# Kernel tuning notes

Measured on AMD Instinct MI355X. Metric: run time of the kernel, lower is better.

Reference implementation:

```python
import jax, jax.numpy as jnp
import numpy as np

H = 16          # num_heads
HD = 64         # head_dim = latent_dim // num_heads
RHD = 32        # rope_head_dim = head_dim // 2
NHD = 32        # nope_head_dim
Q_LAT = 256     # latent_dim // compression_ratio
KV_LAT = 204    # xf_latent_dim // (compression_ratio + 1)
MAX_LEN = 2048
THETA = 10000.0
EPS = 1e-5


def _rope_tables():
    half = RHD // 2  # 16
    freqs = 1.0 / THETA ** (np.arange(half, dtype=np.float32) / half)
    t = np.arange(MAX_LEN, dtype=np.float32)
    ang = np.outer(t, freqs)  # (MAX_LEN, half)
    return jnp.asarray(np.cos(ang)), jnp.asarray(np.sin(ang))

COS, SIN = _rope_tables()


def _ln(x, g, b):
    m = jnp.mean(x, axis=-1, keepdims=True)
    v = jnp.var(x, axis=-1, keepdims=True)
    return (x - m) * jax.lax.rsqrt(v + EPS) * g + b


def _rope(t, cos, sin):
    # t: (..., L, RHD); cos/sin: (L, RHD//2); interleaved even/odd convention
    ev, od = t[..., 0::2], t[..., 1::2]
    oe = ev * cos - od * sin
    oo = ev * sin + od * cos
    return jnp.stack([oe, oo], axis=-1).reshape(t.shape)


def setup_inputs() -> dict:
    key = jax.random.key(0)
    ks = jax.random.split(key, 12)
    D = 1024
    s = 0.02
    return {
        "x": jax.random.normal(ks[0], (2, 2048, D), jnp.float32),
        "xf": jax.random.normal(ks[1], (2, 2048, D), jnp.float32),
        "Wqc": jax.random.normal(ks[2], (D, Q_LAT), jnp.float32) * s,
        "gq": jnp.ones((Q_LAT,), jnp.float32),
        "bq": jnp.zeros((Q_LAT,), jnp.float32),
        "Wq_rope": jax.random.normal(ks[3], (Q_LAT, H * RHD), jnp.float32) * s,
        "Wq_nope": jax.random.normal(ks[4], (Q_LAT, H * NHD), jnp.float32) * s,
        "Wkvc": jax.random.normal(ks[5], (D, KV_LAT), jnp.float32) * s,
        "gkv": jnp.ones((KV_LAT,), jnp.float32),
        "bkv": jnp.zeros((KV_LAT,), jnp.float32),
        "Wk_nope": jax.random.normal(ks[6], (KV_LAT, H * NHD), jnp.float32) * s,
        "Wv": jax.random.normal(ks[7], (KV_LAT, H * HD), jnp.float32) * s,
        "Wkr": jax.random.normal(ks[8], (D, RHD), jnp.float32) * s,
        "Wo": jax.random.normal(ks[9], (D, D), jnp.float32) * s,
        "bo": jnp.zeros((D,), jnp.float32),
    }


def reference(x, xf, Wqc, gq, bq, Wq_rope, Wq_nope, Wkvc, gkv, bkv, Wk_nope, Wv, Wkr, Wo, bo):
    B, T, D = x.shape
    S = xf.shape[1]

    # query path: compress -> LN -> decoupled decompress
    ql = _ln(x @ Wqc, gq, bq)                                   # (B,T,Q_LAT)
    q_nope = (ql @ Wq_nope).reshape(B, T, H, NHD).transpose(0, 2, 1, 3)  # (B,H,T,NHD)
    q_rope = (ql @ Wq_rope).reshape(B, T, H, RHD).transpose(0, 2, 1, 3)  # (B,H,T,RHD)

    # key/value path: compress -> LN -> decompress; shared single rope head
    kvl = _ln(xf @ Wkvc, gkv, bkv)                              # (B,S,KV_LAT)
    k_nope = (kvl @ Wk_nope).reshape(B, S, H, NHD).transpose(0, 2, 1, 3)  # (B,H,S,NHD)
    v = (kvl @ Wv).reshape(B, S, H, HD).transpose(0, 2, 1, 3)   # (B,H,S,HD)
    k_rope = (xf @ Wkr).reshape(B, S, 1, RHD).transpose(0, 2, 1, 3)       # (B,1,S,RHD)

    q_rope = _rope(q_rope, COS[:T], SIN[:T])
    k_rope = _rope(k_rope, COS[:S], SIN[:S]) / H
    k_rope = jnp.broadcast_to(k_rope, (B, H, S, RHD))

    q = jnp.concatenate([q_nope, q_rope], axis=-1)              # (B,H,T,HD)
    k = jnp.concatenate([k_nope, k_rope], axis=-1)              # (B,H,S,HD)

    scale = 1.0 / jnp.sqrt(jnp.asarray(HD, q.dtype))
    scores = jnp.einsum("bhtd,bhsd->bhts", q, k) * scale
    attn = jax.nn.softmax(scores, axis=-1)
    o = jnp.einsum("bhts,bhsd->bhtd", attn, v)                  # (B,H,T,HD)
    o = o.transpose(0, 2, 1, 3).reshape(B, T, H * HD)
    return o @ Wo + bo
```

## Files before the change

### kernel.cpp

```cpp
#include <hip/hip_runtime.h>
#include <hip/hip_bf16.h>
#include <math.h>

#define SEQ 2048

typedef __bf16 bf16x8 __attribute__((ext_vector_type(8)));
typedef float  f32x4  __attribute__((ext_vector_type(4)));

#if __has_builtin(__builtin_amdgcn_exp2f)
#define EXP2(x) __builtin_amdgcn_exp2f(x)
#else
#define EXP2(x) exp2f(x)
#endif

__device__ __forceinline__ unsigned short f2bf(float f) {
  __bf16 h = (__bf16)f;
  return __builtin_bit_cast(unsigned short, h);
}

__device__ __forceinline__ void gload16(const unsigned short* g, unsigned short* l) {
  __builtin_amdgcn_global_load_lds(
      (const __attribute__((address_space(1))) void*)g,
      (__attribute__((address_space(3))) void*)l, 16, 0, 0);
}

__device__ __forceinline__ unsigned cvtpk(float lo, float hi) {
  unsigned r;
  asm("v_cvt_pk_bf16_f32 %0, %1, %2" : "=v"(r) : "v"(lo), "v"(hi));
  return r;
}
__device__ __forceinline__ void plswap32(unsigned &a, unsigned &b) {
  asm("v_permlane32_swap_b32 %0, %1" : "+v"(a), "+v"(b));
}
__device__ __forceinline__ void plswap16(unsigned &a, unsigned &b) {
  asm("v_permlane16_swap_b32 %0, %1" : "+v"(a), "+v"(b));
}

#define CLOG (0.125f * 1.44269504f)

struct WPrep {
  const float* src[8];
  unsigned short* dst[8];
  int K[8], N[8], NR[8], KC[8], nb[8];
  float2* cst;
};

__global__ __launch_bounds__(256) void wprep_kernel(WPrep p)
{
  __shared__ float tile[32][33];
  int bid = blockIdx.x;
  if (bid < 128) {
    const int idx = bid * 256 + threadIdx.x;
    const int pos = idx >> 4, i = idx & 15;
    const float freq = EXP2(-(float)i * 0.8304820237f);
    const float ang = (float)pos * freq;
    p.cst[idx] = make_float2(cosf(ang), sinf(ang));
    return;
  }
  bid -= 128;
  int di = 0;
  while (bid >= p.nb[di]) { bid -= p.nb[di]; ++di; }
  const float* src = p.src[di];
  unsigned short* dst = p.dst[di];
  const int K = p.K[di], N = p.N[di], KC = p.KC[di];
  const int nkx = KC >> 5;
  const int k0 = (bid % nkx) * 32, n0 = (bid / nkx) * 32;
  const int tx = threadIdx.x & 31, ty = threadIdx.x >> 5;
  for (int r = ty; r < 32; r += 8) {
    const int k = k0 + r, n = n0 + tx;
    tile[r][tx] = (k < K && n < N) ? src[(long)k * N + n] : 0.0f;
  }
  __syncthreads();
  for (int r = ty; r < 32; r += 8) {
    const int n = n0 + r, k = k0 + tx;
    dst[(long)n * KC + k] = f2bf(tile[tx][r]);
  }
}

template <int EPI, bool AF32>
__device__ __forceinline__ void gemm_body(
    unsigned short* smem,
    const void* __restrict__ Av, const unsigned short* __restrict__ BT,
    const float* __restrict__ bias, const float2* __restrict__ cst,
    void* __restrict__ C0v, void* __restrict__ C1v, int K, int N,
    int bx, int by)
{
  unsigned short* As = smem;
  unsigned short* Bs = smem + 2 * 128 * 32;
  const int tid = threadIdx.x;
  const int w = tid >> 6, lane = tid & 63;
  const int ln16 = lane & 15, quad = lane >> 4;
  const int wm = (w >> 1) * 64, wn = (w & 1) * 64;
  const int m0 = by * 128, n0 = bx * 128;
  const int rr = tid >> 2, cc = (tid & 3) * 8;

  const unsigned short* A = (const unsigned short*)Av;

  auto stageB = [&](int ib, int k0) {
    gload16(&BT[(long)(n0 + rr)      * K + k0 + cc], &Bs[ib * 4096 + rr * 32 + cc]);
    gload16(&BT[(long)(n0 + 64 + rr) * K + k0 + cc], &Bs[ib * 4096 + (64 + rr) * 32 + cc]);
  };
  auto stageAbf = [&](int ib, int k0) {
    gload16(&A[(long)(m0 + rr)      * K + k0 + cc], &As[ib * 4096 + rr * 32 + cc]);
    gload16(&A[(long)(m0 + 64 + rr) * K + k0 + cc], &As[ib * 4096 + (64 + rr) * 32 + cc]);
  };

  f32x4 acc[4][4];
#pragma unroll
  for (int i = 0; i < 4; ++i)
#pragma unroll
    for (int j = 0; j < 4; ++j)
#pragma unroll
      for (int r = 0; r < 4; ++r) acc[i][j][r] = 0.0f;

  stageB(0, 0);
  stageAbf(0, 0);

  int ib = 0;
  for (int k0 = 0; k0 < K; k0 += 32, ib ^= 1) {
    __syncthreads();
    const int kn = k0 + 32;
    if (kn < K) { stageB(ib ^ 1, kn); stageAbf(ib ^ 1, kn); }
    bf16x8 fa[4], fb[4];
#pragma unroll
    for (int i = 0; i < 4; ++i) fa[i] = *(const bf16x8*)&As[ib * 4096 + (wm + i * 16 + ln16) * 32 + quad * 8];
#pragma unroll
    for (int j = 0; j < 4; ++j) fb[j] = *(const bf16x8*)&Bs[ib * 4096 + (wn + j * 16 + ln16) * 32 + quad * 8];
#pragma unroll
    for (int i = 0; i < 4; ++i)
#pragma unroll
      for (int j = 0; j < 4; ++j)
        acc[i][j] = __builtin_amdgcn_mfma_f32_16x16x32_bf16(fa[i], fb[j], acc[i][j], 0, 0, 0);
  }

  if (EPI == 5 && n0 >= 512) {
    __syncthreads();
#pragma unroll
    for (int i = 0; i < 4; ++i) {
      const int rl = wm + i * 16 + quad * 4;
#pragma unroll
      for (int j = 0; j < 4; ++j) {
        const int cl = wn + j * 16 + ln16;
        ushort4 u;
        u.x = f2bf(acc[i][j][0]); u.y = f2bf(acc[i][j][1]);
        u.z = f2bf(acc[i][j][2]); u.w = f2bf(acc[i][j][3]);
        *(ushort4*)&smem[cl * 132 + rl] = u;
      }
    }
    __syncthreads();
    unsigned short* vT = (unsigned short*)C1v;
    const int b = m0 >> 11, sbase = m0 & (SEQ - 1);
    for (int q = tid; q < 128 * 16; q += 256) {
      const int cl = q >> 4, sch = (q & 15) * 8;
      bf16x8 val = *(const bf16x8*)&smem[cl * 132 + sch];
      const int c = (n0 - 512) + cl;
      const int hh = c >> 6, dd = c & 63;
      *(bf16x8*)&vT[((long)(b * 16 + hh) * 64 + dd) * SEQ + sbase + sch] = val;
    }
    return;
  }
#pragma unroll
  for (int i = 0; i < 4; ++i) {
    const int row0 = m0 + wm + i * 16 + quad * 4;
#pragma unroll
    for (int j = 0; j < 4; ++j) {
      const int col = n0 + wn + j * 16 + ln16;
      if (EPI == 3) {
        if (n0 < 512) {
          unsigned short* qn = (unsigned short*)C0v;
#pragma unroll
          for (int r = 0; r < 4; ++r) qn[(long)(row0 + r) * 512 + col] = f2bf(acc[i][j][r] * CLOG);
        } else {
          unsigned short* qr = (unsigned short*)C1v;
          const int c = col - 512;
          const int d = c & 31;
#pragma unroll
          for (int r = 0; r < 4; ++r) {
            const float v = acc[i][j][r];
            const float p = __shfl_xor(v, 1);
            const float2 t = cst[((row0 + r) & (SEQ - 1)) * 16 + (d >> 1)];
            const float o = ((d & 1) == 0) ? (v * t.x - p * t.y) : (p * t.y + v * t.x);
            qr[(long)(row0 + r) * 512 + c] = f2bf(o * CLOG);
          }
        }
      } else if (EPI == 5) {
        unsigned short* kn = (unsigned short*)C0v;
#pragma unroll
        for (int r = 0; r < 4; ++r) kn[(long)(row0 + r) * 512 + col] = f2bf(acc[i][j][r]);
      }
    }
  }
}

template <int E0, bool AF0, int E1, bool AF1>
__global__ __launch_bounds__(256) void gemm_dual(
    const void* __restrict__ A0, const unsigned short* __restrict__ BT0,
    void* __restrict__ C00, void* __restrict__ C01, int K0, int N0, int nx0,
    const void* __restrict__ A1, const unsigned short* __restrict__ BT1,
    void* __restrict__ C10, void* __restrict__ C11, int K1, int N1,
    const float2* __restrict__ cst)
{
  __shared__ unsigned short smem[16896];
  if (blockIdx.z == 0) {
    if ((int)blockIdx.x >= nx0) return;
    gemm_body<E0, AF0>(smem, A0, BT0, nullptr, cst, C00, C01, K0, N0, blockIdx.x, blockIdx.y);
  } else {
    gemm_body<E1, AF1>(smem, A1, BT1, nullptr, cst, C10, C11, K1, N1, blockIdx.x, blockIdx.y);
  }
}

template <int EPI, bool AF32>
__device__ __forceinline__ void gemm_body64(
    unsigned short* smem,
    const void* __restrict__ Av, const unsigned short* __restrict__ BT,
    const float* __restrict__ bias, const float2* __restrict__ cst,
    void* __restrict__ C0v, void* __restrict__ C1v, int K, int N,
    int bx, int by)
{
  unsigned short* As = smem;
  unsigned short* Bs = smem + 2 * 64 * 32;
  const int tid = threadIdx.x;
  const int w = tid >> 6, lane = tid & 63;
  const int ln16 = lane & 15, quad = lane >> 4;
  const int wm = (w >> 1) * 32, wn = (w & 1) * 32;
  const int m0 = by * 64, n0 = bx * 64;
  const int rr = tid >> 2, cc = (tid & 3) * 8;

  const unsigned short* A = (const unsigned short*)Av;
  const float* Af = (const float*)Av;

  auto stageB = [&](int ib, int k0) {
    gload16(&BT[(long)(n0 + rr) * K + k0 + cc], &Bs[ib * 2048 + rr * 32 + cc]);
  };
  auto stageAbf = [&](int ib, int k0) {
    gload16(&A[(long)(m0 + rr) * K + k0 + cc], &As[ib * 2048 + rr * 32 + cc]);
  };
  auto writeAf32 = [&](int ib, const float4& a0, const float4& a1) {
    ushort4 u;
    u.x = f2bf(a0.x); u.y = f2bf(a0.y); u.z = f2bf(a0.z); u.w = f2bf(a0.w);
    *(ushort4*)&As[ib * 2048 + rr * 32 + cc] = u;
    u.x = f2bf(a1.x); u.y = f2bf(a1.y); u.z = f2bf(a1.z); u.w = f2bf(a1.w);
    *(ushort4*)&As[ib * 2048 + rr * 32 + cc + 4] = u;
  };

  f32x4 acc[2][2];
#pragma unroll
  for (int i = 0; i < 2; ++i)
#pragma unroll
    for (int j = 0; j < 2; ++j)
#pragma unroll
      for (int r = 0; r < 4; ++r) acc[i][j][r] = 0.0f;

  stageB(0, 0);
  if (AF32) {
    float4 a0 = *(const float4*)&Af[(long)(m0 + rr) * K + cc];
    float4 a1 = *(const float4*)&Af[(long)(m0 + rr) * K + cc + 4];
    writeAf32(0, a0, a1);
  } else {
    stageAbf(0, 0);
  }

  int ib = 0;
  for (int k0 = 0; k0 < K; k0 += 32, ib ^= 1) {
    __syncthreads();
    const int kn = k0 + 32;
    float4 a0, a1;
    if (kn < K) {
      stageB(ib ^ 1, kn);
      if (AF32) {
        a0 = *(const float4*)&Af[(long)(m0 + rr) * K + kn + cc];
        a1 = *(const float4*)&Af[(long)(m0 + rr) * K + kn + cc + 4];
      } else {
        stageAbf(ib ^ 1, kn);
      }
    }
    bf16x8 fa[2], fb[2];
#pragma unroll
    for (int i = 0; i < 2; ++i) fa[i] = *(const bf16x8*)&As[ib * 2048 + (wm + i * 16 + ln16) * 32 + quad * 8];
#pragma unroll
    for (int j = 0; j < 2; ++j) fb[j] = *(const bf16x8*)&Bs[ib * 2048 + (wn + j * 16 + ln16) * 32 + quad * 8];
#pragma unroll
    for (int i = 0; i < 2; ++i)
#pragma unroll
      for (int j = 0; j < 2; ++j)
        acc[i][j] = __builtin_amdgcn_mfma_f32_16x16x32_bf16(fa[i], fb[j], acc[i][j], 0, 0, 0);
    if (AF32 && kn < K) writeAf32(ib ^ 1, a0, a1);
  }

#pragma unroll
  for (int i = 0; i < 2; ++i) {
    const int row0 = m0 + wm + i * 16 + quad * 4;
#pragma unroll
    for (int j = 0; j < 2; ++j) {
      const int col = n0 + wn + j * 16 + ln16;
      if (EPI == 0 || EPI == 1) {
        float* C = (float*)C0v;
        float bv = (EPI == 1) ? bias[col] : 0.0f;
#pragma unroll
        for (int r = 0; r < 4; ++r) C[(long)(row0 + r) * N + col] = acc[i][j][r] + bv;
      } else if (EPI == 4) {
        if (n0 < 256) {
          float* kvl = (float*)C0v;
#pragma unroll
          for (int r = 0; r < 4; ++r) kvl[(long)(row0 + r) * 256 + col] = acc[i][j][r];
        } else if (wn == 0) {
          unsigned short* kr = (unsigned short*)C1v;
          const int d = col - 256;
#pragma unroll
          for (int r = 0; r < 4; ++r) {
            const float v = acc[i][j][r];
            const float p = __shfl_xor(v, 1);
            const float2 t = cst[((row0 + r) & (SEQ - 1)) * 16 + (d >> 1)];
            const float o = ((d & 1) == 0) ? (v * t.x - p * t.y) : (p * t.y + v * t.x);
            kr[(long)(row0 + r) * 32 + d] = f2bf(o * 0.0625f);
          }
        }
      }
    }
  }
}

template <int EPI, bool AF32>
__global__ __launch_bounds__(256) void gemm_mfma64(
    const void* __restrict__ Av, const unsigned short* __restrict__ BT,
    const float* __restrict__ bias, const float2* __restrict__ cst,
    void* __restrict__ C0v, void* __restrict__ C1v, int K, int N)
{
  __shared__ unsigned short smem[8192];
  gemm_body64<EPI, AF32>(smem, Av, BT, bias, cst, C0v, C1v, K, N, blockIdx.x, blockIdx.y);
}

template <int E0, bool AF0, int E1, bool AF1>
__global__ __launch_bounds__(256) void gemm_dual64(
    const void* __restrict__ A0, const unsigned short* __restrict__ BT0,
    void* __restrict__ C00, void* __restrict__ C01, int K0, int N0, int nx0,
    const void* __restrict__ A1, const unsigned short* __restrict__ BT1,
    void* __restrict__ C10, void* __restrict__ C11, int K1, int N1,
    const float2* __restrict__ cst)
{
  __shared__ unsigned short smem[8192];
  if (blockIdx.z == 0) {
    if ((int)blockIdx.x >= nx0) return;
    gemm_body64<E0, AF0>(smem, A0, BT0, nullptr, cst, C00, C01, K0, N0, blockIdx.x, blockIdx.y);
  } else {
    gemm_body64<E1, AF1>(smem, A1, BT1, nullptr, cst, C10, C11, K1, N1, blockIdx.x, blockIdx.y);
  }
}

__global__ __launch_bounds__(256) void ln2_kernel(
    const float* __restrict__ Xq, const float* __restrict__ Xkv,
    const float* __restrict__ gq, const float* __restrict__ bq,
    const float* __restrict__ gkv, const float* __restrict__ bkv,
    unsigned short* __restrict__ Yq, unsigned short* __restrict__ Ykv)
{
  const int row0 = blockIdx.x, tid = threadIdx.x;
  const bool isq = row0 < 4096;
  const int row = isq ? row0 : row0 - 4096;
  const float* X = isq ? Xq : Xkv;
  const float* g = isq ? gq : gkv;
  const float* b = isq ? bq : bkv;
  unsigned short* Y = isq ? Yq : Ykv;
  const int C = isq ? 256 : 204;
  const int Cp = isq ? 256 : 224;
  float v = (tid < C) ? X[(long)row * 256 + tid] : 0.0f;
  float s1 = v, s2 = v * v;
#pragma unroll
  for (int off = 1; off < 64; off <<= 1) {
    s1 += __shfl_xor(s1, off);
    s2 += __shfl_xor(s2, off);
  }
  __shared__ float rA[4], rB[4];
  const int wid = tid >> 6;
  if ((tid & 63) == 0) { rA[wid] = s1; rB[wid] = s2; }
  __syncthreads();
  s1 = rA[0] + rA[1] + rA[2] + rA[3];
  s2 = rB[0] + rB[1] + rB[2] + rB[3];
  const float mean = s1 / C;
  const float var  = s2 / C - mean * mean;
  const float r = rsqrtf(var + 1e-5f);
  if (tid < C) Y[(long)row * Cp + tid] = f2bf((v - mean) * r * g[tid] + b[tid]);
  else if (tid < Cp) Y[(long)row * Cp + tid] = 0;
}

#define KSTR 36
#define VSTR 68
__global__ __launch_bounds__(256, 4) void attn_mfma_kernel(
    const unsigned short* __restrict__ qn, const unsigned short* __restrict__ qr,
    const unsigned short* __restrict__ kn, const unsigned short* __restrict__ kr,
    const unsigned short* __restrict__ vT, unsigned short* __restrict__ ob)
{
  __shared__ unsigned short Kn[2][64 * KSTR];
  __shared__ unsigned short Vs[2][64 * VSTR];
  const int id = blockIdx.x;
  const int xcd = id & 7, j = id >> 3;
  const int bh = xcd * 4 + (j & 3);
  const int tile = j >> 2;
  const int b = bh >> 4, h = bh & 15;
  const int t0 = tile * 64;
  const int tid = threadIdx.x;
  const int w = tid >> 6, lane = tid & 63;
  const int ln16 = lane & 15, quad = lane >> 4;
  const int trow = w * 16;
  const long bT = (long)b * SEQ;

  const int krow = tid >> 2, kc8 = (tid & 3) * 8;
  const int vd0 = tid >> 3, vc0 = (tid & 7) * 8;
  const int vd1 = vd0 + 32;

  bf16x8 q0 = *(const bf16x8*)&qn[(bT + t0 + trow + ln16) * 512 + h * 32 + quad * 8];
  bf16x8 q1 = *(const bf16x8*)&qr[(bT + t0 + trow + ln16) * 512 + h * 32 + quad * 8];

  auto loadKV = [&](int s0, bf16x8& rk0, bf16x8& rv0, bf16x8& rv1) {
    rk0 = *(const bf16x8*)&kn[(bT + s0 + krow) * 512 + h * 32 + kc8];
    rv0 = *(const bf16x8*)&vT[((long)bh * 64 + vd0) * SEQ + s0 + vc0];
    rv1 = *(const bf16x8*)&vT[((long)bh * 64 + vd1) * SEQ + s0 + vc0];
  };
  auto writeKV = [&](int ib, bf16x8 rk0, bf16x8 rv0, bf16x8 rv1) {
    *(bf16x8*)&Kn[ib][krow * KSTR + kc8] = rk0;
    *(bf16x8*)&Vs[ib][vd0 * VSTR + vc0] = rv0;
    *(bf16x8*)&Vs[ib][vd1 * VSTR + vc0] = rv1;
  };
  auto loadKrF = [&](int s0, bf16x8* f) {
#pragma unroll
    for (int nt = 0; nt < 4; ++nt)
      f[nt] = *(const bf16x8*)&kr[(bT + s0 + nt * 16 + ln16) * 32 + quad * 8];
  };

  bf16x8 ck0, cv0, cv1;
  bf16x8 nk0, nv0, nv1;
  bf16x8 ckr[4], nkr[4];
  loadKV(0, ck0, cv0, cv1);
  writeKV(0, ck0, cv0, cv1);
  loadKV(64, nk0, nv0, nv1);
  loadKrF(0, ckr);
  loadKrF(64, nkr);

  f32x4 o_acc[4];
#pragma unroll
  for (int nt = 0; nt < 4; ++nt)
#pragma unroll
    for (int r = 0; r < 4; ++r) o_acc[nt][r] = 0.0f;
  float l_part = 0.0f;

  int ib = 0;
  for (int s0 = 0; s0 < SEQ; s0 += 64, ib ^= 1) {
    __syncthreads();
    if (s0 + 64 < SEQ) {
      writeKV(ib ^ 1, nk0, nv0, nv1);
      if (s0 + 128 < SEQ) loadKV(s0 + 128, nk0, nv0, nv1);
    }

    f32x4 sf[4];
#pragma unroll
    for (int nt = 0; nt < 4; ++nt)
#pragma unroll
      for (int r = 0; r < 4; ++r) sf[nt][r] = 0.0f;
#pragma unroll
    for (int nt = 0; nt < 4; ++nt) {
      bf16x8 a0 = *(const bf16x8*)&Kn[ib][(nt * 16 + ln16) * KSTR + quad * 8];
      sf[nt] = __builtin_amdgcn_mfma_f32_16x16x32_bf16(a0, q0, sf[nt], 0, 0, 0);
      sf[nt] = __builtin_amdgcn_mfma_f32_16x16x32_bf16(ckr[nt], q1, sf[nt], 0, 0, 0);
    }

#pragma unroll
    for (int nt = 0; nt < 4; ++nt) ckr[nt] = nkr[nt];
    if (s0 + 128 < SEQ) loadKrF(s0 + 128, nkr);

    unsigned u0, u1, u2, u3, u4, u5, u6, u7;
    {
      float p[16];
#pragma unroll
      for (int nt = 0; nt < 4; ++nt)
#pragma unroll
        for (int r = 0; r < 4; ++r) {
          const float e = EXP2(sf[nt][r]);
          p[nt * 4 + r] = e;
          l_part += e;
        }
      u0 = cvtpk(p[0],  p[1]);   u1 = cvtpk(p[2],  p[3]);
      u2 = cvtpk(p[4],  p[5]);   u3 = cvtpk(p[6],  p[7]);
      u4 = cvtpk(p[8],  p[9]);   u5 = cvtpk(p[10], p[11]);
      u6 = cvtpk(p[12], p[13]);  u7 = cvtpk(p[14], p[15]);
    }
    plswap32(u0, u2); plswap16(u0, u2);
    plswap32(u1, u3); plswap16(u1, u3);
    plswap32(u4, u6); plswap16(u4, u6);
    plswap32(u5, u7); plswap16(u5, u7);
    const uint4 w0 = make_uint4(u0, u1, u2, u3);
    const uint4 w1 = make_uint4(u4, u5, u6, u7);
    bf16x8 a0 = __builtin_bit_cast(bf16x8, w0);
    bf16x8 a1 = __builtin_bit_cast(bf16x8, w1);

#pragma unroll
    for (int nt = 0; nt < 4; ++nt) {
      bf16x8 v0 = *(const bf16x8*)&Vs[ib][(nt * 16 + ln16) * VSTR + quad * 8];
      o_acc[nt] = __builtin_amdgcn_mfma_f32_16x16x32_bf16(a0, v0, o_acc[nt], 0, 0, 0);
      bf16x8 v1 = *(const bf16x8*)&Vs[ib][(nt * 16 + ln16) * VSTR + 32 + quad * 8];
      o_acc[nt] = __builtin_amdgcn_mfma_f32_16x16x32_bf16(a1, v1, o_acc[nt], 0, 0, 0);
    }
  }

  float l_i = l_part;
  l_i += __shfl_xor(l_i, 16);
  l_i += __shfl_xor(l_i, 32);
  const float lr = 1.0f / l_i;
  float lq[4];
#pragma unroll
  for (int r = 0; r < 4; ++r) lq[r] = __shfl(lr, quad * 4 + r);
#pragma unroll
  for (int r = 0; r < 4; ++r) {
    const long t = t0 + trow + quad * 4 + r;
    const long base = (bT + t) * 1024 + h * 64 + ln16;
#pragma unroll
    for (int nt = 0; nt < 4; ++nt)
      ob[base + nt * 16] = f2bf(o_acc[nt][r] * lq[r]);
  }
}

extern "C" void kernel_launch(void* const* d_in, const int* in_sizes, int n_in,
                              void* d_out, int out_size, void* d_ws, size_t ws_size,
                              hipStream_t stream) {
  const float* x       = (const float*)d_in[0];
  const float* xf      = (const float*)d_in[1];
  const float* Wqc     = (const float*)d_in[2];
  const float* gq      = (const float*)d_in[3];
  const float* bq      = (const float*)d_in[4];
  const float* Wq_rope = (const float*)d_in[5];
  const float* Wq_nope = (const float*)d_in[6];
  const float* Wkvc    = (const float*)d_in[7];
  const float* gkv     = (const float*)d_in[8];
  const float* bkv     = (const float*)d_in[9];
  const float* Wk_nope = (const float*)d_in[10];
  const float* Wv      = (const float*)d_in[11];
  const float* Wkr     = (const float*)d_in[12];
  const float* Wo      = (const float*)d_in[13];
  const float* bo      = (const float*)d_in[14];
  float* out = (float*)d_out;

  const long R = 4096;
  float* ws = (float*)d_ws;
  float* ql_f  = ws;
  float* kvl_f = ql_f + R * 256;
  float2* cst  = (float2*)(kvl_f + R * 256);
  unsigned short* us = (unsigned short*)(cst + 2048 * 16);
  unsigned short* ql_bf  = us;  us += R * 256;
  unsigned short* kvl_bf = us;  us += R * 224;
  unsigned short* qn_bf  = us;  us += R * 512;
  unsigned short* qr_bf  = us;  us += R * 512;
  unsigned short* kn_bf  = us;  us += R * 512;
  unsigned short* kr_bf  = us;  us += R * 32;
  unsigned short* vT_bf  = us;  us += R * 1024;
  unsigned short* o_bf   = us;  us += R * 1024;
  unsigned short* WqcT   = us;  us += 256 * 1024;
  unsigned short* WkvkrT = us;  us += 384 * 1024;
  unsigned short* WqnqrT = us;  us += 1024 * 256;
  unsigned short* WknvT  = us;  us += 1536 * 224;
  unsigned short* WoT    = us;  us += 1024 * 1024;

  WPrep p;
  const float* srcs[8] = {Wqc, Wkvc, Wkr, Wq_nope, Wq_rope, Wk_nope, Wv, Wo};
  unsigned short* dsts[8] = {WqcT, WkvkrT, WkvkrT + 256 * 1024,
                             WqnqrT, WqnqrT + 512 * 256,
                             WknvT, WknvT + 512 * 224, WoT};
  const int Ks[8]  = {1024, 1024, 1024, 256, 256, 204, 204, 1024};
  const int Ns[8]  = {256, 204, 32, 512, 512, 512, 1024, 1024};
  const int NRs[8] = {256, 256, 128, 512, 512, 512, 1024, 1024};
  const int KCs[8] = {1024, 1024, 1024, 256, 256, 224, 224, 1024};
  int total = 128;
  for (int i = 0; i < 8; ++i) {
    p.src[i] = srcs[i]; p.dst[i] = dsts[i];
    p.K[i] = Ks[i]; p.N[i] = Ns[i]; p.NR[i] = NRs[i]; p.KC[i] = KCs[i];
    p.nb[i] = (KCs[i] / 32) * (NRs[i] / 32);
    total += p.nb[i];
  }
  p.cst = cst;
  wprep_kernel<<<total, 256, 0, stream>>>(p);

  gemm_dual64<0, true, 4, true><<<dim3(6, 64, 2), 256, 0, stream>>>(
      x, WqcT, ql_f, nullptr, 1024, 256, 4,
      xf, WkvkrT, kvl_f, kr_bf, 1024, 384, cst);
  ln2_kernel<<<8192, 256, 0, stream>>>(ql_f, kvl_f, gq, bq, gkv, bkv, ql_bf, kvl_bf);
  gemm_dual<3, false, 5, false><<<dim3(12, 32, 2), 256, 0, stream>>>(
      ql_bf, WqnqrT, qn_bf, qr_bf, 256, 1024, 8,
      kvl_bf, WknvT, kn_bf, vT_bf, 224, 1536, cst);
  attn_mfma_kernel<<<1024, 256, 0, stream>>>(qn_bf, qr_bf, kn_bf, kr_bf, vT_bf, o_bf);
  gemm_mfma64<1, false><<<dim3(16, 64), 256, 0, stream>>>(o_bf, WoT, bo, nullptr, out, nullptr, 1024, 1024);
}
```

Before: 232.1 us.

## Process two query tiles per attention block to reuse K/V loads

Each attention block now handles 128 query rows (two 64-row groups) instead of 64, so every K/V tile staged in shared memory and every Kr fragment is reused for twice the MFMA work. Grid size is halved to 512 blocks and launch bounds are relaxed to 2 waves per SIMD to allow the doubled accumulator and score registers. The Kr prefetch is simplified to a single-buffer reload after the score MFMAs. Fewer blocks and higher register pressure lower occupancy and latency hiding in exchange for halved K/V traffic.

Result: faster. 224.0 us (-3.5%).

```diff
diff --git a/kernel.cpp b/kernel.cpp
--- a/kernel.cpp
+++ b/kernel.cpp
@@ -384,7 +384,7 @@
 
 #define KSTR 36
 #define VSTR 68
-__global__ __launch_bounds__(256, 4) void attn_mfma_kernel(
+__global__ __launch_bounds__(256, 2) void attn_mfma_kernel(
     const unsigned short* __restrict__ qn, const unsigned short* __restrict__ qr,
     const unsigned short* __restrict__ kn, const unsigned short* __restrict__ kr,
     const unsigned short* __restrict__ vT, unsigned short* __restrict__ ob)
@@ -396,7 +396,7 @@
   const int bh = xcd * 4 + (j & 3);
   const int tile = j >> 2;
   const int b = bh >> 4, h = bh & 15;
-  const int t0 = tile * 64;
+  const int t0 = tile * 128;
   const int tid = threadIdx.x;
   const int w = tid >> 6, lane = tid & 63;
   const int ln16 = lane & 15, quad = lane >> 4;
@@ -407,8 +407,10 @@
   const int vd0 = tid >> 3, vc0 = (tid & 7) * 8;
   const int vd1 = vd0 + 32;
 
-  bf16x8 q0 = *(const bf16x8*)&qn[(bT + t0 + trow + ln16) * 512 + h * 32 + quad * 8];
-  bf16x8 q1 = *(const bf16x8*)&qr[(bT + t0 + trow + ln16) * 512 + h * 32 + quad * 8];
+  bf16x8 q0A = *(const bf16x8*)&qn[(bT + t0 + trow + ln16) * 512 + h * 32 + quad * 8];
+  bf16x8 q1A = *(const bf16x8*)&qr[(bT + t0 + trow + ln16) * 512 + h * 32 + quad * 8];
+  bf16x8 q0B = *(const bf16x8*)&qn[(bT + t0 + 64 + trow + ln16) * 512 + h * 32 + quad * 8];
+  bf16x8 q1B = *(const bf16x8*)&qr[(bT + t0 + 64 + trow + ln16) * 512 + h * 32 + quad * 8];
 
   auto loadKV = [&](int s0, bf16x8& rk0, bf16x8& rv0, bf16x8& rv1) {
     rk0 = *(const bf16x8*)&kn[(bT + s0 + krow) * 512 + h * 32 + kc8];
@@ -425,22 +427,46 @@
     for (int nt = 0; nt < 4; ++nt)
       f[nt] = *(const bf16x8*)&kr[(bT + s0 + nt * 16 + ln16) * 32 + quad * 8];
   };
+  auto pxform = [&](const f32x4* sf, float& l_part, bf16x8& a0, bf16x8& a1) {
+    float p[16];
+#pragma unroll
+    for (int nt = 0; nt < 4; ++nt)
+#pragma unroll
+      for (int r = 0; r < 4; ++r) {
+        const float e = EXP2(sf[nt][r]);
+        p[nt * 4 + r] = e;
+        l_part += e;
+      }
+    unsigned u0 = cvtpk(p[0],  p[1]),  u1 = cvtpk(p[2],  p[3]);
+    unsigned u2 = cvtpk(p[4],  p[5]),  u3 = cvtpk(p[6],  p[7]);
+    unsigned u4 = cvtpk(p[8],  p[9]),  u5 = cvtpk(p[10], p[11]);
+    unsigned u6 = cvtpk(p[12], p[13]), u7 = cvtpk(p[14], p[15]);
+    plswap32(u0, u2); plswap16(u0, u2);
+    plswap32(u1, u3); plswap16(u1, u3);
+    plswap32(u4, u6); plswap16(u4, u6);
+    plswap32(u5, u7); plswap16(u5, u7);
+    const uint4 w0 = make_uint4(u0, u1, u2, u3);
+    const uint4 w1 = make_uint4(u4, u5, u6, u7);
+    a0 = __builtin_bit_cast(bf16x8, w0);
+    a1 = __builtin_bit_cast(bf16x8, w1);
+  };
 
   bf16x8 ck0, cv0, cv1;
   bf16x8 nk0, nv0, nv1;
-  bf16x8 ckr[4], nkr[4];
+  bf16x8 ckr[4];
   loadKV(0, ck0, cv0, cv1);
   writeKV(0, ck0, cv0, cv1);
   loadKV(64, nk0, nv0, nv1);
   loadKrF(0, ckr);
-  loadKrF(64, nkr);
-
-  f32x4 o_acc[4];
-#pragma unroll
-  for (int nt = 0; nt < 4; ++nt)
-#pragma unroll
-    for (int r = 0; r < 4; ++r) o_acc[nt][r] = 0.0f;
-  float l_part = 0.0f;
+
+  f32x4 o_acc[2][4];
+#pragma unroll
+  for (int g = 0; g < 2; ++g)
+#pragma unroll
+    for (int nt = 0; nt < 4; ++nt)
+#pragma unroll
+      for (int r = 0; r < 4; ++r) o_acc[g][nt][r] = 0.0f;
+  float l_part[2] = {0.0f, 0.0f};
 
   int ib = 0;
   for (int s0 = 0; s0 < SEQ; s0 += 64, ib ^= 1) {
@@ -450,70 +476,61 @@
       if (s0 + 128 < SEQ) loadKV(s0 + 128, nk0, nv0, nv1);
     }
 
-    f32x4 sf[4];
+    bf16x8 ka[4];
 #pragma unroll
     for (int nt = 0; nt < 4; ++nt)
-#pragma unroll
-      for (int r = 0; r < 4; ++r) sf[nt][r] = 0.0f;
+      ka[nt] = *(const bf16x8*)&Kn[ib][(nt * 16 + ln16) * KSTR + quad * 8];
+
+    f32x4 sfA[4], sfB[4];
+#pragma unroll
+    for (int nt = 0; nt < 4; ++nt)
+#pragma unroll
+      for (int r = 0; r < 4; ++r) { sfA[nt][r] = 0.0f; sfB[nt][r] = 0.0f; }
 #pragma unroll
     for (int nt = 0; nt < 4; ++nt) {
-      bf16x8 a0 = *(const bf16x8*)&Kn[ib][(nt * 16 + ln16) * KSTR + quad * 8];
-      sf[nt] = __builtin_amdgcn_mfma_f32_16x16x32_bf16(a0, q0, sf[nt], 0, 0, 0);
-      sf[nt] = __builtin_amdgcn_mfma_f32_16x16x32_bf16(ckr[nt], q1, sf[nt], 0, 0, 0);
-    }
-
-#pragma unroll
-    for (int nt = 0; nt < 4; ++nt) ckr[nt] = nkr[nt];
-    if (s0 + 128 < SEQ) loadKrF(s0 + 128, nkr);
-
-    unsigned u0, u1, u2, u3, u4, u5, u6, u7;
-    {
-      float p[16];
-#pragma unroll
-      for (int nt = 0; nt < 4; ++nt)
-#pragma unroll
-        for (int r = 0; r < 4; ++r) {
-          const float e = EXP2(sf[nt][r]);
-          p[nt * 4 + r] = e;
-          l_part += e;
-        }
-      u0 = cvtpk(p[0],  p[1]);   u1 = cvtpk(p[2],  p[3]);
-      u2 = cvtpk(p[4],  p[5]);   u3 = cvtpk(p[6],  p[7]);
-      u4 = cvtpk(p[8],  p[9]);   u5 = cvtpk(p[10], p[11]);
-      u6 = cvtpk(p[12], p[13]);  u7 = cvtpk(p[14], p[15]);
-    }
-    plswap32(u0, u2); plswap16(u0, u2);
-    plswap32(u1, u3); plswap16(u1, u3);
-    plswap32(u4, u6); plswap16(u4, u6);
-    plswap32(u5, u7); plswap16(u5, u7);
-    const uint4 w0 = make_uint4(u0, u1, u2, u3);
-    const uint4 w1 = make_uint4(u4, u5, u6, u7);
-    bf16x8 a0 = __builtin_bit_cast(bf16x8, w0);
-    bf16x8 a1 = __builtin_bit_cast(bf16x8, w1);
+      sfA[nt] = __builtin_amdgcn_mfma_f32_16x16x32_bf16(ka[nt], q0A, sfA[nt], 0, 0, 0);
+      sfA[nt] = __builtin_amdgcn_mfma_f32_16x16x32_bf16(ckr[nt], q1A, sfA[nt], 0, 0, 0);
+    }
+#pragma unroll
+    for (int nt = 0; nt < 4; ++nt) {
+      sfB[nt] = __builtin_amdgcn_mfma_f32_16x16x32_bf16(ka[nt], q0B, sfB[nt], 0, 0, 0);
+      sfB[nt] = __builtin_amdgcn_mfma_f32_16x16x32_bf16(ckr[nt], q1B, sfB[nt], 0, 0, 0);
+    }
+
+    if (s0 + 64 < SEQ) loadKrF(s0 + 64, ckr);
+
+    bf16x8 a0A, a1A, a0B, a1B;
+    pxform(sfA, l_part[0], a0A, a1A);
+    pxform(sfB, l_part[1], a0B, a1B);
 
 #pragma unroll
     for (int nt = 0; nt < 4; ++nt) {
       bf16x8 v0 = *(const bf16x8*)&Vs[ib][(nt * 16 + ln16) * VSTR + quad * 8];
-      o_acc[nt] = __builtin_amdgcn_mfma_f32_16x16x32_bf16(a0, v0, o_acc[nt], 0, 0, 0);
+      o_acc[0][nt] = __builtin_amdgcn_mfma_f32_16x16x32_bf16(a0A, v0, o_acc[0][nt], 0, 0, 0);
+      o_acc[1][nt] = __builtin_amdgcn_mfma_f32_16x16x32_bf16(a0B, v0, o_acc[1][nt], 0, 0, 0);
       bf16x8 v1 = *(const bf16x8*)&Vs[ib][(nt * 16 + ln16) * VSTR + 32 + quad * 8];
-      o_acc[nt] = __builtin_amdgcn_mfma_f32_16x16x32_bf16(a1, v1, o_acc[nt], 0, 0, 0);
-    }
-  }
-
-  float l_i = l_part;
-  l_i += __shfl_xor(l_i, 16);
-  l_i += __shfl_xor(l_i, 32);
-  const float lr = 1.0f / l_i;
-  float lq[4];
-#pragma unroll
-  for (int r = 0; r < 4; ++r) lq[r] = __shfl(lr, quad * 4 + r);
-#pragma unroll
-  for (int r = 0; r < 4; ++r) {
-    const long t = t0 + trow + quad * 4 + r;
-    const long base = (bT + t) * 1024 + h * 64 + ln16;
-#pragma unroll
-    for (int nt = 0; nt < 4; ++nt)
-      ob[base + nt * 16] = f2bf(o_acc[nt][r] * lq[r]);
+      o_acc[0][nt] = __builtin_amdgcn_mfma_f32_16x16x32_bf16(a1A, v1, o_acc[0][nt], 0, 0, 0);
+      o_acc[1][nt] = __builtin_amdgcn_mfma_f32_16x16x32_bf16(a1B, v1, o_acc[1][nt], 0, 0, 0);
+    }
+  }
+
+#pragma unroll
+  for (int g = 0; g < 2; ++g) {
+    float l_i = l_part[g];
+    l_i += __shfl_xor(l_i, 16);
+    l_i += __shfl_xor(l_i, 32);
+    const float lr = 1.0f / l_i;
+    float lq[4];
+#pragma unroll
+    for (int r = 0; r < 4; ++r) lq[r] = __shfl(lr, quad * 4 + r);
+#pragma unroll
+    for (int r = 0; r < 4; ++r) {
+      const long t = t0 + g * 64 + trow + quad * 4 + r;
+      const long base = (bT + t) * 1024 + h * 64 + ln16;
+#pragma unroll
+      for (int nt = 0; nt < 4; ++nt)
+        ob[base + nt * 16] = f2bf(o_acc[g][nt][r] * lq[r]);
+    }
   }
 }
 
@@ -583,6 +600,6 @@
   gemm_dual<3, false, 5, false><<<dim3(12, 32, 2), 256, 0, stream>>>(
       ql_bf, WqnqrT, qn_bf, qr_bf, 256, 1024, 8,
       kvl_bf, WknvT, kn_bf, vT_bf, 224, 1536, cst);
-  attn_mfma_kernel<<<1024, 256, 0, stream>>>(qn_bf, qr_bf, kn_bf, kr_bf, vT_bf, o_bf);
+  attn_mfma_kernel<<<512, 256, 0, stream>>>(qn_bf, qr_bf, kn_bf, kr_bf, vT_bf, o_bf);
   gemm_mfma64<1, false><<<dim3(16, 64), 256, 0, stream>>>(o_bf, WoT, bo, nullptr, out, nullptr, 1024, 1024);
 }
```
